# Kernel tuning notes

Measured on AMD Instinct MI355X. Metric: run time of the kernel, lower is better.

The kernel has to match this reference:

```python
import jax, jax.numpy as jnp
import numpy as np

MIN_SCORE = 0.3       # min_score_threshold
NMS_THRESHOLD = 0.3   # nms_threshold
MAX_OUT = 256         # fixed output padding (jit-compatible replacement for dynamic K)


def _cxcywh_to_xyxy(b):
    cx, cy, w, h = b[..., 0], b[..., 1], b[..., 2], b[..., 3]
    half_w, half_h = w * 0.5, h * 0.5
    return jnp.stack([cx - half_w, cy - half_h, cx + half_w, cy + half_h], axis=-1)


def _pairwise_iou(a, b):
    # a: [N,4], b: [M,4] in xyxy
    lt = jnp.maximum(a[:, None, :2], b[None, :, :2])
    rb = jnp.minimum(a[:, None, 2:], b[None, :, 2:])
    wh = jnp.clip(rb - lt, 0.0)
    inter = wh[..., 0] * wh[..., 1]
    area_a = (a[:, 2] - a[:, 0]) * (a[:, 3] - a[:, 1])
    area_b = (b[:, 2] - b[:, 0]) * (b[:, 3] - b[:, 1])
    return inter / (area_a[:, None] + area_b[None, :] - inter + 1e-9)


def setup_inputs() -> dict:
    key = jax.random.key(0)
    k1, k2 = jax.random.split(key)
    N, n_coords = 8192, 16
    score = jax.random.uniform(k1, (N, 1), dtype=jnp.float32)
    box = jax.random.uniform(k2, (N, n_coords), dtype=jnp.float32)
    return {"score": score, "box": box}


def reference(score, box):
    # score: [N,1], box: [N,n_coords]; single class (n_classes==1, cls=None)
    s = score[:, 0]
    valid = s >= MIN_SCORE                      # score mask applied before NMS
    order = jnp.argsort(-s)                     # score-descending (batched_nms order)
    s_s = s[order]
    v_s = valid[order]
    box_s = box[order]
    bbox = _cxcywh_to_xyxy(box_s[:, :4]).astype(jnp.float32)
    iou = _pairwise_iou(bbox, bbox)             # [N,N]
    N = s.shape[0]

    def body(kept, i):
        # suppressed if overlaps any already-kept (higher-score) box
        suppressed = jnp.any(kept & (iou[:, i] > NMS_THRESHOLD))
        keep_i = v_s[i] & jnp.logical_not(suppressed)
        return kept.at[i].set(keep_i), None

    kept, _ = jax.lax.scan(body, jnp.zeros((N,), dtype=bool), jnp.arange(N))

    # compact kept detections to the front, preserving score order (stable sort)
    comp = jnp.argsort(jnp.where(kept, 0, 1), stable=True)[:MAX_OUT]
    out_valid = kept[comp]                      # [MAX_OUT]
    score_out = jnp.where(out_valid[:, None], s_s[comp][:, None], 0.0)   # [MAX_OUT,1]
    box_out = jnp.where(out_valid[:, None], box_s[comp], 0.0)            # [MAX_OUT,n_coords]
    return score_out, box_out, out_valid
```

## Files before the change

### kernel.cpp

```cpp
#include <hip/hip_runtime.h>
#include <stdint.h>

typedef unsigned long long u64;

#define N 8192
#define NW 128
#define MAX_OUT 256
#define MASK_BYTES ((size_t)N * NW * 8)


__global__ __launch_bounds__(256)
void build_keys_kernel(const float* __restrict__ score, u64* __restrict__ keys,
                       int* __restrict__ rank, int* __restrict__ partial) {
    int i = blockIdx.x * 256 + threadIdx.x;
    float s = score[i];
    uint32_t b = __float_as_uint(s);
    keys[i] = ((u64)(~b) << 32) | (uint32_t)i;
    rank[i] = 0;
    int c = (s >= 0.3f) ? 1 : 0;
    for (int off = 32; off; off >>= 1) c += __shfl_down(c, off);
    __shared__ int part[4];
    if ((threadIdx.x & 63) == 0) part[threadIdx.x >> 6] = c;
    __syncthreads();
    if (threadIdx.x == 0) partial[blockIdx.x] = part[0] + part[1] + part[2] + part[3];
}

__global__ __launch_bounds__(256)
void rank_kernel(const u64* __restrict__ keys, int* __restrict__ rank,
                 const int* __restrict__ partial, int* __restrict__ nvalid) {
    __shared__ u64 kj[1024];
    const int tid = threadIdx.x;
    if (blockIdx.x == 0 && blockIdx.y == 0 && tid < 64) {
        int v = (tid < 32) ? partial[tid] : 0;
        for (int off = 32; off; off >>= 1) v += __shfl_down(v, off);
        if (tid == 0) *nvalid = v;
    }
    const int jbase = blockIdx.y * 1024;
    for (int t = tid; t < 1024; t += 256) kj[t] = keys[jbase + t];
    __syncthreads();
    const int i = blockIdx.x * 256 + tid;
    const u64 ki = keys[i];
    int c = 0;
    #pragma unroll 8
    for (int j = 0; j < 1024; ++j) c += (kj[j] < ki) ? 1 : 0;
    atomicAdd(&rank[i], c);
}

__global__ __launch_bounds__(256)
void scatter_kernel(const float* __restrict__ score, const float* __restrict__ box,
                    const int* __restrict__ rank, int* __restrict__ order,
                    float* __restrict__ s_s, float4* __restrict__ bbox,
                    float* __restrict__ area) {
    int i = blockIdx.x * 256 + threadIdx.x;
    int r = rank[i];
    float s = score[i];
    order[r] = i;
    s_s[r] = s;
    float4 cb = ((const float4*)box)[i * 4];
    float hw = cb.z * 0.5f, hh = cb.w * 0.5f;
    float x0 = cb.x - hw, y0 = cb.y - hh, x1 = cb.x + hw, y1 = cb.y + hh;
    bbox[r] = make_float4(x0, y0, x1, y1);
    area[r] = (x1 - x0) * (y1 - y0);
}

__global__ __launch_bounds__(256)
void mask_kernel(const float4* __restrict__ bbox, const float* __restrict__ area,
                 const int* __restrict__ nvalid_p, u64* __restrict__ mask) {
    const int w = blockIdx.x;
    const int i = blockIdx.y * 256 + threadIdx.x;
    __shared__ float4 jb[64];
    __shared__ float  ja[64];
    if (threadIdx.x < 64) {
        jb[threadIdx.x] = bbox[w * 64 + threadIdx.x];
        ja[threadIdx.x] = area[w * 64 + threadIdx.x];
    }
    __syncthreads();
    const int nv = *nvalid_p;
    if (i >= nv) return;
    if (w < (i >> 6)) return;
    float4 a = bbox[i];
    float  aa = area[i];
    u64 bits = 0;
    #pragma unroll 8
    for (int jj = 0; jj < 64; ++jj) {
        float4 b = jb[jj];
        float lx = fmaxf(a.x, b.x), ly = fmaxf(a.y, b.y);
        float rx = fminf(a.z, b.z), ry = fminf(a.w, b.w);
        float ww = fmaxf(rx - lx, 0.0f), hh = fmaxf(ry - ly, 0.0f);
        float inter = ww * hh;
        float denom = ((aa + ja[jj]) - inter) + 1e-9f;
        float iou = inter / denom;
        bits |= ((u64)(iou > 0.3f)) << jj;
    }
    mask[(size_t)i * NW + w] = bits;
}


struct Pipe { u64 col, s1, s2, g0, g1, g2, g3; };

__device__ __forceinline__ unsigned or_dpp32(unsigned v) {
    v |= (unsigned)__builtin_amdgcn_update_dpp(0, (int)v, 0x111, 0xf, 0xf, true);
    v |= (unsigned)__builtin_amdgcn_update_dpp(0, (int)v, 0x112, 0xf, 0xf, true);
    v |= (unsigned)__builtin_amdgcn_update_dpp(0, (int)v, 0x114, 0xf, 0xf, true);
    v |= (unsigned)__builtin_amdgcn_update_dpp(0, (int)v, 0x118, 0xf, 0xf, true);
    v |= (unsigned)__builtin_amdgcn_update_dpp(0, (int)v, 0x142, 0xf, 0xf, true);
    v |= (unsigned)__builtin_amdgcn_update_dpp(0, (int)v, 0x143, 0xf, 0xf, true);
    return v;
}

__device__ __forceinline__ u64 wave_or64(u64 v) {
    unsigned lo = or_dpp32((unsigned)v);
    unsigned hi = or_dpp32((unsigned)(v >> 32));
    unsigned slo = (unsigned)__builtin_amdgcn_readlane((int)lo, 63);
    unsigned shi = (unsigned)__builtin_amdgcn_readlane((int)hi, 63);
    return ((u64)shi << 32) | (u64)slo;
}

__global__ __launch_bounds__(64)
void nms_kernel(const u64* __restrict__ mask, const float* __restrict__ s_s,
                const int* __restrict__ order, const float* __restrict__ box,
                const int* __restrict__ nvalid_p, float* __restrict__ out) {
    const int lane = threadIdx.x;
    const int nv = *nvalid_p;
    const int nblk = (nv + 63) >> 6;
    __shared__ int kpos[MAX_OUT];
    int kcount = 0;
    u64 s1m = 0, s2m = 0, s2m_old = 0;

    Pipe A, B;
    A.col = A.s1 = A.s2 = A.g0 = A.g1 = A.g2 = A.g3 = 0;
    B.col = B.s1 = B.s2 = B.g0 = B.g1 = B.g2 = B.g3 = 0;
    if (nblk > 0) {
        const u64* r = mask + (size_t)lane * NW;
        A.col = r[0];
        if (nblk > 1) A.s1 = r[1];
        if (nblk > 2) A.s2 = r[2];
    }
    if (nblk > 1) {
        const u64* r = mask + (size_t)(64 + lane) * NW;
        B.col = r[1];
        if (nblk > 2) B.s1 = r[2];
        if (nblk > 3) B.s2 = r[3];
    }

    auto step = [&](int b, Pipe& P) -> bool {
        u64 col = P.col, s1v = P.s1, s2v = P.s2;
        u64 x = P.g0 | P.g1 | P.g2 | P.g3 | s1m | s2m_old;
        const int b2 = b + 2;
        P.col = P.s1 = P.s2 = P.g0 = P.g1 = P.g2 = P.g3 = 0;
        if (b2 < nblk) {
            const u64* r = mask + (size_t)((b2 << 6) + lane) * NW;
            P.col = r[b2];
            if (b2 + 1 < nblk) P.s1 = r[b2 + 1];
            if (b2 + 2 < nblk) P.s2 = r[b2 + 2];
            const int kc = kcount;
            if (lane < kc)       P.g0 = mask[(size_t)kpos[lane]       * NW + b2];
            if (lane +  64 < kc) P.g1 = mask[(size_t)kpos[lane +  64] * NW + b2];
            if (lane + 128 < kc) P.g2 = mask[(size_t)kpos[lane + 128] * NW + b2];
            if (lane + 192 < kc) P.g3 = mask[(size_t)kpos[lane + 192] * NW + b2];
        }
        u64 rw = wave_or64(x);
        const int base = b << 6;
        const int rem = nv - base;
        u64 validm = (rem >= 64) ? ~0ull : ((1ull << rem) - 1ull);
        u64 todo = validm & ~rw;
        u64 km = 0;
        while (todo) {
            int l = (int)__builtin_ctzll(todo);
            u64 row_l = __ballot(((col >> l) & 1ull) != 0);
            if (lane == 0) kpos[kcount] = base + l;
            km |= (1ull << l);
            kcount++;
            todo &= ~row_l;
            todo &= ~(1ull << l);
            if (kcount >= MAX_OUT) break;
        }
        u64 keepm = ((km >> lane) & 1ull) ? ~0ull : 0ull;
        s2m_old = s2m;
        s2m = s2v & keepm;
        s1m = s1v & keepm;
        return kcount < MAX_OUT;
    };

    bool run = true;
    for (int b = 0; run && b < nblk; b += 2) {
        run = step(b, A);
        if (run && b + 1 < nblk) run = step(b + 1, B);
    }

    __syncthreads();
    float* out_score = out;
    float* out_box   = out + MAX_OUT;
    float* out_valid = out + MAX_OUT + MAX_OUT * 16;
    const float4* box4 = (const float4*)box;
    float4* ob4 = (float4*)out_box;
    for (int t = lane; t < MAX_OUT; t += 64) {
        if (t < kcount) {
            int p = kpos[t];
            out_score[t] = s_s[p];
            out_valid[t] = 1.0f;
            int oi = order[p];
            #pragma unroll
            for (int q = 0; q < 4; ++q) ob4[t * 4 + q] = box4[oi * 4 + q];
        } else {
            out_score[t] = 0.0f;
            out_valid[t] = 0.0f;
            float4 z = make_float4(0.f, 0.f, 0.f, 0.f);
            #pragma unroll
            for (int q = 0; q < 4; ++q) ob4[t * 4 + q] = z;
        }
    }
}

extern "C" void kernel_launch(void* const* d_in, const int* in_sizes, int n_in,
                              void* d_out, int out_size, void* d_ws, size_t ws_size,
                              hipStream_t stream) {
    const float* score = (const float*)d_in[0];
    const float* box   = (const float*)d_in[1];
    char* ws = (char*)d_ws;
    u64*    mask    = (u64*)ws;
    u64*    keys    = (u64*)ws;
    int*    rank    = (int*)(ws + 65536);
    int*    partial = (int*)(ws + 98304);
    int*    order  = (int*)   (ws + MASK_BYTES);
    float*  s_s    = (float*) (ws + MASK_BYTES + 32768);
    float4* bbox   = (float4*)(ws + MASK_BYTES + 65536);
    float*  area   = (float*) (ws + MASK_BYTES + 65536 + 131072);
    int*    nvalid = (int*)   (ws + MASK_BYTES + 65536 + 131072 + 32768);

    build_keys_kernel<<<32, 256, 0, stream>>>(score, keys, rank, partial);
    rank_kernel<<<dim3(32, 8), 256, 0, stream>>>(keys, rank, partial, nvalid);
    scatter_kernel<<<32, 256, 0, stream>>>(score, box, rank, order, s_s, bbox, area);
    mask_kernel<<<dim3(128, 32), 256, 0, stream>>>(bbox, area, nvalid, mask);
    nms_kernel<<<1, 64, 0, stream>>>(mask, s_s, order, box, nvalid, (float*)d_out);
}
```

Baseline: 139.1 us.

## Fuse key, rank, scatter and mask stages into one cooperative kernel

```diff
diff --git a/kernel.cpp b/kernel.cpp
--- a/kernel.cpp
+++ b/kernel.cpp
@@ -1,6 +1,8 @@
 #include <hip/hip_runtime.h>
+#include <hip/hip_cooperative_groups.h>
 #include <stdint.h>
 
+namespace cg = cooperative_groups;
 typedef unsigned long long u64;
 
 #define N 8192
@@ -10,91 +12,98 @@
 
 
 __global__ __launch_bounds__(256)
-void build_keys_kernel(const float* __restrict__ score, u64* __restrict__ keys,
-                       int* __restrict__ rank, int* __restrict__ partial) {
-    int i = blockIdx.x * 256 + threadIdx.x;
-    float s = score[i];
-    uint32_t b = __float_as_uint(s);
-    keys[i] = ((u64)(~b) << 32) | (uint32_t)i;
-    rank[i] = 0;
-    int c = (s >= 0.3f) ? 1 : 0;
-    for (int off = 32; off; off >>= 1) c += __shfl_down(c, off);
-    __shared__ int part[4];
-    if ((threadIdx.x & 63) == 0) part[threadIdx.x >> 6] = c;
-    __syncthreads();
-    if (threadIdx.x == 0) partial[blockIdx.x] = part[0] + part[1] + part[2] + part[3];
-}
-
-__global__ __launch_bounds__(256)
-void rank_kernel(const u64* __restrict__ keys, int* __restrict__ rank,
-                 const int* __restrict__ partial, int* __restrict__ nvalid) {
-    __shared__ u64 kj[1024];
+void front_kernel(const float* __restrict__ score, const float* __restrict__ box,
+                  int* __restrict__ partial16, u64* __restrict__ mask,
+                  int* __restrict__ order, float* __restrict__ s_s,
+                  float4* __restrict__ bbox, float* __restrict__ area,
+                  int* __restrict__ nvalid) {
+    cg::grid_group gridg = cg::this_grid();
     const int tid = threadIdx.x;
-    if (blockIdx.x == 0 && blockIdx.y == 0 && tid < 64) {
-        int v = (tid < 32) ? partial[tid] : 0;
-        for (int off = 32; off; off >>= 1) v += __shfl_down(v, off);
-        if (tid == 0) *nvalid = v;
-    }
-    const int jbase = blockIdx.y * 1024;
-    for (int t = tid; t < 1024; t += 256) kj[t] = keys[jbase + t];
-    __syncthreads();
-    const int i = blockIdx.x * 256 + tid;
-    const u64 ki = keys[i];
-    int c = 0;
-    #pragma unroll 8
-    for (int j = 0; j < 1024; ++j) c += (kj[j] < ki) ? 1 : 0;
-    atomicAdd(&rank[i], c);
-}
-
-__global__ __launch_bounds__(256)
-void scatter_kernel(const float* __restrict__ score, const float* __restrict__ box,
-                    const int* __restrict__ rank, int* __restrict__ order,
-                    float* __restrict__ s_s, float4* __restrict__ bbox,
-                    float* __restrict__ area) {
-    int i = blockIdx.x * 256 + threadIdx.x;
-    int r = rank[i];
-    float s = score[i];
-    order[r] = i;
-    s_s[r] = s;
-    float4 cb = ((const float4*)box)[i * 4];
-    float hw = cb.z * 0.5f, hh = cb.w * 0.5f;
-    float x0 = cb.x - hw, y0 = cb.y - hh, x1 = cb.x + hw, y1 = cb.y + hh;
-    bbox[r] = make_float4(x0, y0, x1, y1);
-    area[r] = (x1 - x0) * (y1 - y0);
-}
-
-__global__ __launch_bounds__(256)
-void mask_kernel(const float4* __restrict__ bbox, const float* __restrict__ area,
-                 const int* __restrict__ nvalid_p, u64* __restrict__ mask) {
-    const int w = blockIdx.x;
-    const int i = blockIdx.y * 256 + threadIdx.x;
+    const int g = blockIdx.x;
+
+    __shared__ u64 kj[512];
     __shared__ float4 jb[64];
     __shared__ float  ja[64];
-    if (threadIdx.x < 64) {
-        jb[threadIdx.x] = bbox[w * 64 + threadIdx.x];
-        ja[threadIdx.x] = area[w * 64 + threadIdx.x];
-    }
-    __syncthreads();
-    const int nv = *nvalid_p;
-    if (i >= nv) return;
-    if (w < (i >> 6)) return;
-    float4 a = bbox[i];
-    float  aa = area[i];
-    u64 bits = 0;
-    #pragma unroll 8
-    for (int jj = 0; jj < 64; ++jj) {
-        float4 b = jb[jj];
-        float lx = fmaxf(a.x, b.x), ly = fmaxf(a.y, b.y);
-        float rx = fminf(a.z, b.z), ry = fminf(a.w, b.w);
-        float ww = fmaxf(rx - lx, 0.0f), hh = fmaxf(ry - ly, 0.0f);
-        float inter = ww * hh;
-        float denom = ((aa + ja[jj]) - inter) + 1e-9f;
-        float iou = inter / denom;
-        bits |= ((u64)(iou > 0.3f)) << jj;
-    }
-    mask[(size_t)i * NW + w] = bits;
-}
-
+    __shared__ int    red[4];
+
+    {
+        const int jc = g >> 5;
+        const int ic = g & 31;
+        const int jbase = jc * 512;
+        const int ibase = ic * 256;
+        for (int t = tid; t < 512; t += 256) {
+            uint32_t sb = __float_as_uint(score[jbase + t]);
+            kj[t] = ((u64)(~sb) << 32) | (uint32_t)(jbase + t);
+        }
+        uint32_t sbi = __float_as_uint(score[ibase + tid]);
+        const u64 ki = ((u64)(~sbi) << 32) | (uint32_t)(ibase + tid);
+        __syncthreads();
+        int c = 0;
+        #pragma unroll 16
+        for (int j = 0; j < 512; ++j) c += (kj[j] < ki) ? 1 : 0;
+        partial16[jc * N + ibase + tid] = c;
+    }
+    __threadfence();
+    gridg.sync();
+
+    if (g < 32) {
+        const int i = g * 256 + tid;
+        int r = 0;
+        #pragma unroll 16
+        for (int k = 0; k < 16; ++k) r += partial16[k * N + i];
+        float s = score[i];
+        order[r] = i;
+        s_s[r] = s;
+        float4 cb = ((const float4*)box)[i * 4];
+        float hw = cb.z * 0.5f, hh = cb.w * 0.5f;
+        float x0 = cb.x - hw, y0 = cb.y - hh, x1 = cb.x + hw, y1 = cb.y + hh;
+        bbox[r] = make_float4(x0, y0, x1, y1);
+        area[r] = (x1 - x0) * (y1 - y0);
+    } else if (g == 32) {
+        int c = 0;
+        for (int i = tid; i < N; i += 256) c += (score[i] >= 0.3f) ? 1 : 0;
+        for (int off = 32; off; off >>= 1) c += __shfl_down(c, off);
+        if ((tid & 63) == 0) red[tid >> 6] = c;
+        __syncthreads();
+        if (tid == 0) *nvalid = red[0] + red[1] + red[2] + red[3];
+    }
+    __threadfence();
+    gridg.sync();
+
+    {
+        const int w = g & 127;
+        const int by0 = g >> 7;
+        const int nv = *nvalid;
+        if (w >= by0 * 4) {
+            if (tid < 64) {
+                jb[tid] = bbox[w * 64 + tid];
+                ja[tid] = area[w * 64 + tid];
+            }
+            __syncthreads();
+            for (int by = by0; by < 32; by += 4) {
+                if (w < by * 4) break;
+                const int i = by * 256 + tid;
+                if (i < nv && w >= (i >> 6)) {
+                    float4 a = bbox[i];
+                    float  aa = area[i];
+                    u64 bits = 0;
+                    #pragma unroll 8
+                    for (int jj = 0; jj < 64; ++jj) {
+                        float4 b = jb[jj];
+                        float lx = fmaxf(a.x, b.x), ly = fmaxf(a.y, b.y);
+                        float rx = fminf(a.z, b.z), ry = fminf(a.w, b.w);
+                        float ww = fmaxf(rx - lx, 0.0f), hh = fmaxf(ry - ly, 0.0f);
+                        float inter = ww * hh;
+                        float denom = ((aa + ja[jj]) - inter) + 1e-9f;
+                        float iou = inter / denom;
+                        bits |= ((u64)(iou > 0.3f)) << jj;
+                    }
+                    mask[(size_t)i * NW + w] = bits;
+                }
+            }
+        }
+    }
+}
 
 struct Pipe { u64 col, s1, s2, g0, g1, g2, g3; };
 
@@ -218,19 +227,19 @@
     const float* score = (const float*)d_in[0];
     const float* box   = (const float*)d_in[1];
     char* ws = (char*)d_ws;
-    u64*    mask    = (u64*)ws;
-    u64*    keys    = (u64*)ws;
-    int*    rank    = (int*)(ws + 65536);
-    int*    partial = (int*)(ws + 98304);
+    u64*    mask      = (u64*)ws;
+    int*    partial16 = (int*)ws;
     int*    order  = (int*)   (ws + MASK_BYTES);
     float*  s_s    = (float*) (ws + MASK_BYTES + 32768);
     float4* bbox   = (float4*)(ws + MASK_BYTES + 65536);
     float*  area   = (float*) (ws + MASK_BYTES + 65536 + 131072);
     int*    nvalid = (int*)   (ws + MASK_BYTES + 65536 + 131072 + 32768);
-
-    build_keys_kernel<<<32, 256, 0, stream>>>(score, keys, rank, partial);
-    rank_kernel<<<dim3(32, 8), 256, 0, stream>>>(keys, rank, partial, nvalid);
-    scatter_kernel<<<32, 256, 0, stream>>>(score, box, rank, order, s_s, bbox, area);
-    mask_kernel<<<dim3(128, 32), 256, 0, stream>>>(bbox, area, nvalid, mask);
-    nms_kernel<<<1, 64, 0, stream>>>(mask, s_s, order, box, nvalid, (float*)d_out);
-}
+    float*  outp   = (float*)d_out;
+
+    void* args[] = {(void*)&score, (void*)&box, (void*)&partial16, (void*)&mask,
+                    (void*)&order, (void*)&s_s, (void*)&bbox, (void*)&area,
+                    (void*)&nvalid};
+    hipLaunchCooperativeKernel((const void*)front_kernel, dim3(512), dim3(256),
+                               args, 0, stream);
+    nms_kernel<<<1, 64, 0, stream>>>(mask, s_s, order, box, nvalid, outp);
+}
```

Measured after the change: 301.9 us. 2.17x slower.
